# Performance work log

Hardware: AMD Instinct MI355X
Metric: run time of the kernel (lower is better)

The kernel has to match this reference:

```python
import jax, jax.numpy as jnp
import numpy as np

N, S, E = 50000, 16, 400000
D, EDIM = 128, 64
H, K = 4, 32          # n_head, per-head output_dim
NMP, DEPTH = 2, 2


def attn_agg(x, neigh, Wq, Wk, Wv):
    # x: [n, D], neigh: [n, s, D], W*: [H, D, K]
    q = jnp.einsum('nd,hdk->nhk', x, Wq)
    k = jnp.einsum('nsd,hdk->nshk', neigh, Wk)
    v = jnp.einsum('nsd,hdk->nshk', neigh, Wv)
    scale = jnp.asarray(1.0 / np.sqrt(K), x.dtype)
    scores = jnp.einsum('nhk,nshk->nhs', q, k) * scale
    attn = jax.nn.softmax(scores, axis=-1)
    out = jax.nn.elu(jnp.einsum('nhs,nshk->nhk', attn, v))  # activation per head
    return out.reshape(out.shape[0], H * K)                  # concat heads


def setup_inputs():
    key = jax.random.key(0)
    ks = jax.random.split(key, 14)
    sD, sE = 1.0 / np.sqrt(D), 1.0 / np.sqrt(EDIM)
    return {
        'feats': jax.random.normal(ks[0], (N, D), jnp.float32),
        'node_emb': jax.random.normal(ks[1], (N, D), jnp.float32) * 0.02,
        'Wprep': jax.random.normal(ks[2], (D, D), jnp.float32) * sD,
        'edge_emb': jax.random.normal(ks[3], (NMP, E, EDIM), jnp.float32),
        'Wedgeprep': jax.random.normal(ks[4], (NMP, EDIM, D), jnp.float32) * sE,
        'Wq_e': jax.random.normal(ks[5], (NMP, DEPTH, H, D, K), jnp.float32) * sD,
        'Wk_e': jax.random.normal(ks[6], (NMP, DEPTH, H, D, K), jnp.float32) * sD,
        'Wv_e': jax.random.normal(ks[7], (NMP, DEPTH, H, D, K), jnp.float32) * sD,
        'Wq_n': jax.random.normal(ks[8], (NMP, DEPTH, H, D, K), jnp.float32) * sD,
        'Wk_n': jax.random.normal(ks[9], (NMP, DEPTH, H, D, K), jnp.float32) * sD,
        'Wv_n': jax.random.normal(ks[10], (NMP, DEPTH, H, D, K), jnp.float32) * sD,
        'node2edge_idx': jax.random.randint(ks[11], (NMP, N, S), 0, E, jnp.int32),
        'edge_node_adj': jax.random.randint(ks[12], (NMP, E, 2), 0, N, jnp.int32),
    }


def reference(feats, node_emb, Wprep, edge_emb, Wedgeprep,
              Wq_e, Wk_e, Wv_e, Wq_n, Wk_n, Wv_n,
              node2edge_idx, edge_node_adj):
    outputs = []
    for mp in range(NMP):
        f = jax.lax.stop_gradient(feats)           # feats[all_ids].detach()
        dummy_feats = node_emb                      # prep layer_idx=0 (id embedding)
        all_feats = f @ Wprep                       # prep layer_idx=1
        all_edges = edge_emb[mp] @ Wedgeprep[mp]    # edge_prep[mp], shuffle=False
        skip = []
        for l in range(DEPTH):
            # --- edge update: gather 2 endpoint node feats per edge ---
            en = all_feats[edge_node_adj[mp]]       # [E, 2, D]
            next_edges = attn_agg(all_edges, en, Wq_e[mp, l], Wk_e[mp, l], Wv_e[mp, l])
            # --- node update: gather S incident edge feats per node (OLD edges) ---
            x = dummy_feats if l == 0 else all_feats
            ne = all_edges[node2edge_idx[mp]]       # [N, S, D]
            next_feats = attn_agg(x, ne, Wq_n[mp, l], Wk_n[mp, l], Wv_n[mp, l])
            skip.append(next_feats)
            all_feats, all_edges = next_feats, next_edges
        outputs.append(jnp.concatenate(skip, axis=-1))  # [N, DEPTH*H*K]
    return jnp.stack(outputs, axis=0)                   # [NMP, N, DEPTH*H*K]
```

## Files before the change

### kernel.cpp

```cpp
#include <hip/hip_runtime.h>

#define N_NODES 50000
#define S_NEI 16
#define E_EDGES 400000
#define DDIM 128
#define EDIMC 64
#define NMPC 2
#define DEPTHC 2

typedef __attribute__((ext_vector_type(8))) short short8v;
typedef __attribute__((ext_vector_type(4))) float float4v;

__device__ __forceinline__ unsigned short f2bf(float f) {
  unsigned int u = __float_as_uint(f);
  unsigned int r = (u + 0x7fffu + ((u >> 16) & 1u)) >> 16;
  return (unsigned short)r;
}
__device__ __forceinline__ float bf2f(unsigned short h) { return __uint_as_float((unsigned int)h << 16); }
__device__ __forceinline__ float bflo(unsigned int u) { return __uint_as_float(u << 16); }
__device__ __forceinline__ float bfhi(unsigned int u) { return __uint_as_float(u & 0xffff0000u); }

__global__ void build_wt(const float* __restrict__ Wprep, const float* __restrict__ Wedgeprep,
                         const float* __restrict__ Wq_e, const float* __restrict__ Wk_e,
                         const float* __restrict__ Wv_e, const float* __restrict__ Wq_n,
                         const float* __restrict__ Wk_n, const float* __restrict__ Wv_n,
                         unsigned short* __restrict__ WT) {
  int idx = blockIdx.x * 256 + threadIdx.x;
  if (idx >= 27 * 16384) return;
  int slot = idx >> 14, r = idx & 16383;
  float v = 0.f;
  if (slot < 24) {
    int ml = slot / 6, mat = slot % 6;
    int c = r >> 7, d = r & 127;
    int h = c >> 5, kk = c & 31;
    const float* W = (mat == 0) ? Wk_e : (mat == 1) ? Wv_e : (mat == 2) ? Wq_n
                   : (mat == 3) ? Wq_e : (mat == 4) ? Wk_n : Wv_n;
    v = W[(((size_t)ml * 4 + h) * 128 + d) * 32 + kk];
  } else if (slot == 24) {
    int c = r >> 7, d = r & 127;
    v = Wprep[d * 128 + c];
  } else {
    int mp = slot - 25;
    int c = r >> 6, k = r & 63;
    if (c < 128) v = Wedgeprep[((size_t)mp * 64 + k) * 128 + c];
  }
  WT[idx] = f2bf(v);
}

template<int KDIM, int NW, bool ASPLIT>
__global__ __launch_bounds__(256, 3)
void proj(const unsigned short* __restrict__ Xbf, const float* __restrict__ Xf,
          const unsigned short* __restrict__ WT,
          unsigned short* __restrict__ Y0, unsigned short* __restrict__ Y1,
          unsigned short* __restrict__ Y2, int rs0, int rs1, int rs2, int M) {
  constexpr int NKK  = KDIM / 32;
  constexpr int CHPR = KDIM / 8;
  constexpr int SWZ  = CHPR - 1;
  __shared__ unsigned short Wl[128 * KDIM];
  const int tid  = threadIdx.x;
  const int lane = tid & 63;
  const int wv   = tid >> 6;
  const int l15  = lane & 15, lg = lane >> 4;
  const long m0  = (long)blockIdx.x * 128 + wv * 32;

  short8v xb[2][NKK];
  #pragma unroll
  for (int rf = 0; rf < 2; ++rf) {
    long row = m0 + rf * 16 + l15; if (row >= M) row = M - 1;
    #pragma unroll
    for (int kk = 0; kk < NKK; ++kk) {
      const int k0 = kk * 32 + lg * 8;
      if (ASPLIT) {
        const float* p = Xf + row * KDIM + k0;
        float4v a0 = *(const float4v*)p;
        float4v a1 = *(const float4v*)(p + 4);
        #pragma unroll
        for (int j = 0; j < 8; ++j) {
          float x = (j < 4) ? a0[j] : a1[j - 4];
          xb[rf][kk][j] = (short)f2bf(x);
        }
      } else {
        xb[rf][kk] = *(const short8v*)(Xbf + row * KDIM + k0);
      }
    }
  }

  unsigned short* Ys[3] = {Y0, Y1, Y2};
  const int rsv[3] = {rs0, rs1, rs2};
  #pragma unroll
  for (int w = 0; w < NW; ++w) {
    if (w) __syncthreads();
    {
      const uint4* src = (const uint4*)(WT + (size_t)w * 16384);
      #pragma unroll
      for (int i = 0; i < CHPR / 2; ++i) {
        int ci = i * 256 + tid;
        int row = ci / CHPR, ch = ci & SWZ;
        uint4 v = src[ci];
        *(uint4*)((char*)Wl + row * (KDIM * 2) + ((ch ^ (row & SWZ)) << 4)) = v;
      }
    }
    __syncthreads();

    float4v acc[8][2];
    #pragma unroll
    for (int cf = 0; cf < 8; ++cf)
      #pragma unroll
      for (int rf = 0; rf < 2; ++rf) acc[cf][rf] = (float4v)0.f;

    #pragma unroll
    for (int kk = 0; kk < NKK; ++kk) {
      #pragma unroll
      for (int cf = 0; cf < 8; ++cf) {
        const int row = cf * 16 + l15;
        const int ch  = (kk * 4 + lg) ^ (row & SWZ);
        short8v b = *(const short8v*)((char*)Wl + row * (KDIM * 2) + (ch << 4));
        acc[cf][0] = __builtin_amdgcn_mfma_f32_16x16x32_bf16(b, xb[0][kk], acc[cf][0], 0, 0, 0);
        acc[cf][1] = __builtin_amdgcn_mfma_f32_16x16x32_bf16(b, xb[1][kk], acc[cf][1], 0, 0, 0);
      }
    }

    #pragma unroll
    for (int rf = 0; rf < 2; ++rf) {
      const long m = m0 + rf * 16 + l15;
      if (m < M) {
        #pragma unroll
        for (int cf = 0; cf < 8; ++cf) {
          const int c0 = cf * 16 + lg * 4;
          float4v a = acc[cf][rf];
          ushort4 o;
          o.x = f2bf(a[0]); o.y = f2bf(a[1]); o.z = f2bf(a[2]); o.w = f2bf(a[3]);
          *(ushort4*)(Ys[w] + m * (long)rsv[w] + c0) = o;
        }
      }
    }
  }
}

__global__ __launch_bounds__(256, 3)
void edge_fused(unsigned short* __restrict__ ehi, const unsigned short* __restrict__ WTqe,
                const unsigned short* __restrict__ KVn, const int* __restrict__ adj,
                unsigned short* __restrict__ KVe) {
  __shared__ unsigned short Wl[128 * 128];
  const int tid  = threadIdx.x;
  const int lane = tid & 63;
  const int wv   = tid >> 6;
  const int l15  = lane & 15, lg = lane >> 4;
  const long m0  = (long)blockIdx.x * 128 + wv * 32;

  short8v xb[2][4];
  #pragma unroll
  for (int rf = 0; rf < 2; ++rf) {
    const long row = m0 + rf * 16 + l15;
    #pragma unroll
    for (int kk = 0; kk < 4; ++kk)
      xb[rf][kk] = *(const short8v*)(ehi + row * 128 + kk * 32 + lg * 8);
  }

  float4v accQ[8][2];
  const int slot_of[3] = {1, 2, 0};
  #pragma unroll
  for (int ph = 0; ph < 3; ++ph) {
    if (ph) __syncthreads();
    {
      const uint4* src = (const uint4*)(WTqe + (size_t)slot_of[ph] * 16384);
      #pragma unroll
      for (int i = 0; i < 8; ++i) {
        int ci = i * 256 + tid;
        int row = ci >> 4, ch = ci & 15;
        uint4 v = src[ci];
        *(uint4*)((char*)Wl + row * 256 + ((ch ^ (row & 15)) << 4)) = v;
      }
    }
    __syncthreads();

    float4v acc[8][2];
    #pragma unroll
    for (int cf = 0; cf < 8; ++cf)
      #pragma unroll
      for (int rf = 0; rf < 2; ++rf) acc[cf][rf] = (float4v)0.f;

    #pragma unroll
    for (int kk = 0; kk < 4; ++kk) {
      #pragma unroll
      for (int cf = 0; cf < 8; ++cf) {
        const int row = cf * 16 + l15;
        const int ch  = (kk * 4 + lg) ^ (row & 15);
        short8v b = *(const short8v*)((char*)Wl + row * 256 + (ch << 4));
        acc[cf][0] = __builtin_amdgcn_mfma_f32_16x16x32_bf16(b, xb[0][kk], acc[cf][0], 0, 0, 0);
        acc[cf][1] = __builtin_amdgcn_mfma_f32_16x16x32_bf16(b, xb[1][kk], acc[cf][1], 0, 0, 0);
      }
    }

    if (ph < 2) {
      #pragma unroll
      for (int rf = 0; rf < 2; ++rf) {
        const long m = m0 + rf * 16 + l15;
        #pragma unroll
        for (int cf = 0; cf < 8; ++cf) {
          const int c0 = cf * 16 + lg * 4;
          float4v a = acc[cf][rf];
          ushort4 o;
          o.x = f2bf(a[0]); o.y = f2bf(a[1]); o.z = f2bf(a[2]); o.w = f2bf(a[3]);
          *(ushort4*)(KVe + m * 256 + ph * 128 + c0) = o;
        }
      }
    } else {
      #pragma unroll
      for (int cf = 0; cf < 8; ++cf)
        #pragma unroll
        for (int rf = 0; rf < 2; ++rf) accQ[cf][rf] = acc[cf][rf];
    }
  }

  const float scale = 0.17677669529663687f;
  #pragma unroll
  for (int rf = 0; rf < 2; ++rf) {
    const long e = m0 + rf * 16 + l15;
    const int2 nn = *(const int2*)(adj + e * 2);
    const size_t b0 = (size_t)nn.x * 256, b1 = (size_t)nn.y * 256;
    float p0[4] = {0.f, 0.f, 0.f, 0.f}, p1[4] = {0.f, 0.f, 0.f, 0.f};
    #pragma unroll
    for (int cf = 0; cf < 8; ++cf) {
      const int c0 = cf * 16 + lg * 4;
      const int h = cf >> 1;
      ushort4 k0 = *(const ushort4*)(KVn + b0 + c0);
      ushort4 k1 = *(const ushort4*)(KVn + b1 + c0);
      float4v q = accQ[cf][rf];
      p0[h] += q[0] * bf2f(k0.x) + q[1] * bf2f(k0.y) + q[2] * bf2f(k0.z) + q[3] * bf2f(k0.w);
      p1[h] += q[0] * bf2f(k1.x) + q[1] * bf2f(k1.y) + q[2] * bf2f(k1.z) + q[3] * bf2f(k1.w);
    }
    float a0[4], a1[4];
    #pragma unroll
    for (int h = 0; h < 4; ++h) {
      p0[h] += __shfl_xor(p0[h], 16); p0[h] += __shfl_xor(p0[h], 32);
      p1[h] += __shfl_xor(p1[h], 16); p1[h] += __shfl_xor(p1[h], 32);
      const float s0 = p0[h] * scale, s1 = p1[h] * scale;
      const float mx = fmaxf(s0, s1);
      const float e0 = __expf(s0 - mx), e1 = __expf(s1 - mx);
      const float inv = 1.0f / (e0 + e1);
      a0[h] = e0 * inv; a1[h] = e1 * inv;
    }
    #pragma unroll
    for (int cf = 0; cf < 8; ++cf) {
      const int c0 = cf * 16 + lg * 4;
      const int h = cf >> 1;
      ushort4 v0 = *(const ushort4*)(KVn + b0 + 128 + c0);
      ushort4 v1 = *(const ushort4*)(KVn + b1 + 128 + c0);
      float o[4];
      o[0] = a0[h] * bf2f(v0.x) + a1[h] * bf2f(v1.x);
      o[1] = a0[h] * bf2f(v0.y) + a1[h] * bf2f(v1.y);
      o[2] = a0[h] * bf2f(v0.z) + a1[h] * bf2f(v1.z);
      o[3] = a0[h] * bf2f(v0.w) + a1[h] * bf2f(v1.w);
      ushort4 ob;
      o[0] = o[0] > 0.f ? o[0] : expm1f(o[0]);
      o[1] = o[1] > 0.f ? o[1] : expm1f(o[1]);
      o[2] = o[2] > 0.f ? o[2] : expm1f(o[2]);
      o[3] = o[3] > 0.f ? o[3] : expm1f(o[3]);
      ob.x = f2bf(o[0]); ob.y = f2bf(o[1]); ob.z = f2bf(o[2]); ob.w = f2bf(o[3]);
      *(ushort4*)(ehi + e * 128 + c0) = ob;
    }
  }
}

__global__ __launch_bounds__(256)
void node_attn(const unsigned int* __restrict__ Qn, const unsigned int* __restrict__ KVe,
               const int* __restrict__ n2e,
               unsigned short* __restrict__ fhi, float* __restrict__ outp) {
  const int lane = threadIdx.x & 63;
  const long n = (long)blockIdx.x * 4 + (threadIdx.x >> 6);
  const unsigned int q = Qn[n * 64 + lane];
  const float qa = bflo(q), qb = bfhi(q);
  float sc[16];
  unsigned int vv[16];
  #pragma unroll
  for (int s = 0; s < 16; ++s) {
    const long e = n2e[n * 16 + s];
    const unsigned int kk = KVe[e * 128 + lane];
    vv[s] = KVe[e * 128 + 64 + lane];
    float p = qa * bflo(kk) + qb * bfhi(kk);
    #pragma unroll
    for (int off = 1; off < 16; off <<= 1) p += __shfl_xor(p, off);
    sc[s] = p * 0.17677669529663687f;
  }
  float m = sc[0];
  #pragma unroll
  for (int s = 1; s < 16; ++s) m = fmaxf(m, sc[s]);
  float sum = 0.f;
  #pragma unroll
  for (int s = 0; s < 16; ++s) { sc[s] = __expf(sc[s] - m); sum += sc[s]; }
  const float inv = 1.0f / sum;
  float oa = 0.f, ob = 0.f;
  #pragma unroll
  for (int s = 0; s < 16; ++s) { oa += sc[s] * bflo(vv[s]); ob += sc[s] * bfhi(vv[s]); }
  oa *= inv; ob *= inv;
  oa = oa > 0.f ? oa : expm1f(oa);
  ob = ob > 0.f ? ob : expm1f(ob);
  ((unsigned int*)fhi)[n * 64 + lane] = (unsigned int)f2bf(oa) | ((unsigned int)f2bf(ob) << 16);
  *(float2*)(outp + n * 256 + lane * 2) = make_float2(oa, ob);
}

extern "C" void kernel_launch(void* const* d_in, const int* in_sizes, int n_in,
                              void* d_out, int out_size, void* d_ws, size_t ws_size,
                              hipStream_t stream) {
  const float* feats     = (const float*)d_in[0];
  const float* node_emb  = (const float*)d_in[1];
  const float* Wprep     = (const float*)d_in[2];
  const float* edge_emb  = (const float*)d_in[3];
  const float* Wedgeprep = (const float*)d_in[4];
  const float* Wq_e      = (const float*)d_in[5];
  const float* Wk_e      = (const float*)d_in[6];
  const float* Wv_e      = (const float*)d_in[7];
  const float* Wq_n      = (const float*)d_in[8];
  const float* Wk_n      = (const float*)d_in[9];
  const float* Wv_n      = (const float*)d_in[10];
  const int*   n2e       = (const int*)d_in[11];
  const int*   adj       = (const int*)d_in[12];
  float* out = (float*)d_out;

  char* w = (char*)d_ws;
  auto carve = [&](size_t bytes) -> char* {
    char* p = w; w += (bytes + 255) & ~(size_t)255; return p;
  };
  unsigned short* ehi  = (unsigned short*)carve((size_t)E_EDGES * 128 * 2);
  unsigned short* fahi = (unsigned short*)carve((size_t)N_NODES * 128 * 2);
  unsigned short* fbhi = (unsigned short*)carve((size_t)N_NODES * 128 * 2);
  unsigned short* KVe  = (unsigned short*)carve((size_t)E_EDGES * 256 * 2);
  unsigned short* KVn  = (unsigned short*)carve((size_t)N_NODES * 256 * 2);
  unsigned short* Qn   = (unsigned short*)carve((size_t)N_NODES * 128 * 2);
  unsigned short* WT   = (unsigned short*)carve((size_t)27 * 16384 * 2);

  build_wt<<<(27 * 16384 + 255) / 256, 256, 0, stream>>>(
      Wprep, Wedgeprep, Wq_e, Wk_e, Wv_e, Wq_n, Wk_n, Wv_n, WT);

  const int gN = (N_NODES + 127) / 128;
  const int gE = E_EDGES / 128;

  for (int mp = 0; mp < NMPC; ++mp) {
    proj<128, 1, true><<<gN, 256, 0, stream>>>(
        nullptr, feats, WT + (size_t)24 * 16384, fahi, nullptr, nullptr, 128, 0, 0, N_NODES);
    proj<64, 1, true><<<gE, 256, 0, stream>>>(
        nullptr, edge_emb + (size_t)mp * E_EDGES * EDIMC,
        WT + (size_t)(25 + mp) * 16384, ehi, nullptr, nullptr, 128, 0, 0, E_EDGES);

    unsigned short *fchi = fahi, *fnhi = fbhi;
    for (int l = 0; l < DEPTHC; ++l) {
      const int ml = mp * 2 + l;
      const unsigned short* base = WT + (size_t)ml * 6 * 16384;
      if (l == 0) {
        proj<128, 2, false><<<gN, 256, 0, stream>>>(
            fchi, nullptr, base, KVn, KVn + 128, nullptr, 256, 256, 0, N_NODES);
        proj<128, 1, true><<<gN, 256, 0, stream>>>(
            nullptr, node_emb, base + (size_t)2 * 16384, Qn, nullptr, nullptr, 128, 0, 0, N_NODES);
      } else {
        proj<128, 3, false><<<gN, 256, 0, stream>>>(
            fchi, nullptr, base, KVn, KVn + 128, Qn, 256, 256, 128, N_NODES);
      }
      edge_fused<<<gE, 256, 0, stream>>>(
          ehi, base + (size_t)3 * 16384, KVn, adj + (size_t)mp * E_EDGES * 2, KVe);
      node_attn<<<N_NODES / 4, 256, 0, stream>>>(
          (const unsigned int*)Qn, (const unsigned int*)KVe,
          n2e + (size_t)mp * N_NODES * S_NEI, fnhi,
          out + (size_t)mp * N_NODES * 256 + (size_t)l * 128);

      unsigned short* t = fchi; fchi = fnhi; fnhi = t;
    }
  }
}
```

Measured before the change: 1.305 ms.

## Split edge kernel into KV-projection and Q-attention block roles with double-buffered edges

The fused edge kernel now launches twice as many blocks: even blocks compute the edge K/V projections and odd blocks compute the Q projection plus the two-endpoint attention. Edge features are ping-ponged between two buffers so the attention blocks can write new edges while the K/V blocks still read the old ones. The node feature prep projection is hoisted out of the message-passing loop into a separate buffer, so it runs once instead of once per mp. This trades one more edge-sized buffer and a duplicated load of the input edge tile for more parallelism and fewer serial phases per block.

Result: slower. 1.556 ms (+19.3%).

```diff
diff --git a/kernel.cpp b/kernel.cpp
--- a/kernel.cpp
+++ b/kernel.cpp
@@ -138,15 +138,16 @@
 }
 
 __global__ __launch_bounds__(256, 3)
-void edge_fused(unsigned short* __restrict__ ehi, const unsigned short* __restrict__ WTqe,
+void edge_layer(const unsigned short* __restrict__ ecur, const unsigned short* __restrict__ WTqe,
                 const unsigned short* __restrict__ KVn, const int* __restrict__ adj,
-                unsigned short* __restrict__ KVe) {
+                unsigned short* __restrict__ KVe, unsigned short* __restrict__ enext) {
   __shared__ unsigned short Wl[128 * 128];
   const int tid  = threadIdx.x;
   const int lane = tid & 63;
   const int wv   = tid >> 6;
   const int l15  = lane & 15, lg = lane >> 4;
-  const long m0  = (long)blockIdx.x * 128 + wv * 32;
+  const int role = blockIdx.x & 1;
+  const long m0  = (long)(blockIdx.x >> 1) * 128 + wv * 32;
 
   short8v xb[2][4];
   #pragma unroll
@@ -154,45 +155,43 @@
     const long row = m0 + rf * 16 + l15;
     #pragma unroll
     for (int kk = 0; kk < 4; ++kk)
-      xb[rf][kk] = *(const short8v*)(ehi + row * 128 + kk * 32 + lg * 8);
-  }
-
-  float4v accQ[8][2];
-  const int slot_of[3] = {1, 2, 0};
-  #pragma unroll
-  for (int ph = 0; ph < 3; ++ph) {
-    if (ph) __syncthreads();
-    {
-      const uint4* src = (const uint4*)(WTqe + (size_t)slot_of[ph] * 16384);
-      #pragma unroll
-      for (int i = 0; i < 8; ++i) {
-        int ci = i * 256 + tid;
-        int row = ci >> 4, ch = ci & 15;
-        uint4 v = src[ci];
-        *(uint4*)((char*)Wl + row * 256 + ((ch ^ (row & 15)) << 4)) = v;
-      }
-    }
-    __syncthreads();
-
-    float4v acc[8][2];
-    #pragma unroll
-    for (int cf = 0; cf < 8; ++cf)
-      #pragma unroll
-      for (int rf = 0; rf < 2; ++rf) acc[cf][rf] = (float4v)0.f;
-
-    #pragma unroll
-    for (int kk = 0; kk < 4; ++kk) {
-      #pragma unroll
-      for (int cf = 0; cf < 8; ++cf) {
-        const int row = cf * 16 + l15;
-        const int ch  = (kk * 4 + lg) ^ (row & 15);
-        short8v b = *(const short8v*)((char*)Wl + row * 256 + (ch << 4));
-        acc[cf][0] = __builtin_amdgcn_mfma_f32_16x16x32_bf16(b, xb[0][kk], acc[cf][0], 0, 0, 0);
-        acc[cf][1] = __builtin_amdgcn_mfma_f32_16x16x32_bf16(b, xb[1][kk], acc[cf][1], 0, 0, 0);
-      }
-    }
-
-    if (ph < 2) {
+      xb[rf][kk] = *(const short8v*)(ecur + row * 128 + kk * 32 + lg * 8);
+  }
+
+  if (role == 0) {
+    #pragma unroll
+    for (int ph = 0; ph < 2; ++ph) {
+      if (ph) __syncthreads();
+      {
+        const uint4* src = (const uint4*)(WTqe + (size_t)(ph + 1) * 16384);
+        #pragma unroll
+        for (int i = 0; i < 8; ++i) {
+          int ci = i * 256 + tid;
+          int row = ci >> 4, ch = ci & 15;
+          uint4 v = src[ci];
+          *(uint4*)((char*)Wl + row * 256 + ((ch ^ (row & 15)) << 4)) = v;
+        }
+      }
+      __syncthreads();
+
+      float4v acc[8][2];
+      #pragma unroll
+      for (int cf = 0; cf < 8; ++cf)
+        #pragma unroll
+        for (int rf = 0; rf < 2; ++rf) acc[cf][rf] = (float4v)0.f;
+
+      #pragma unroll
+      for (int kk = 0; kk < 4; ++kk) {
+        #pragma unroll
+        for (int cf = 0; cf < 8; ++cf) {
+          const int row = cf * 16 + l15;
+          const int ch  = (kk * 4 + lg) ^ (row & 15);
+          short8v b = *(const short8v*)((char*)Wl + row * 256 + (ch << 4));
+          acc[cf][0] = __builtin_amdgcn_mfma_f32_16x16x32_bf16(b, xb[0][kk], acc[cf][0], 0, 0, 0);
+          acc[cf][1] = __builtin_amdgcn_mfma_f32_16x16x32_bf16(b, xb[1][kk], acc[cf][1], 0, 0, 0);
+        }
+      }
+
       #pragma unroll
       for (int rf = 0; rf < 2; ++rf) {
         const long m = m0 + rf * 16 + l15;
@@ -205,11 +204,37 @@
           *(ushort4*)(KVe + m * 256 + ph * 128 + c0) = o;
         }
       }
-    } else {
-      #pragma unroll
-      for (int cf = 0; cf < 8; ++cf)
-        #pragma unroll
-        for (int rf = 0; rf < 2; ++rf) accQ[cf][rf] = acc[cf][rf];
+    }
+    return;
+  }
+
+  {
+    const uint4* src = (const uint4*)WTqe;
+    #pragma unroll
+    for (int i = 0; i < 8; ++i) {
+      int ci = i * 256 + tid;
+      int row = ci >> 4, ch = ci & 15;
+      uint4 v = src[ci];
+      *(uint4*)((char*)Wl + row * 256 + ((ch ^ (row & 15)) << 4)) = v;
+    }
+  }
+  __syncthreads();
+
+  float4v accQ[8][2];
+  #pragma unroll
+  for (int cf = 0; cf < 8; ++cf)
+    #pragma unroll
+    for (int rf = 0; rf < 2; ++rf) accQ[cf][rf] = (float4v)0.f;
+
+  #pragma unroll
+  for (int kk = 0; kk < 4; ++kk) {
+    #pragma unroll
+    for (int cf = 0; cf < 8; ++cf) {
+      const int row = cf * 16 + l15;
+      const int ch  = (kk * 4 + lg) ^ (row & 15);
+      short8v b = *(const short8v*)((char*)Wl + row * 256 + (ch << 4));
+      accQ[cf][0] = __builtin_amdgcn_mfma_f32_16x16x32_bf16(b, xb[0][kk], accQ[cf][0], 0, 0, 0);
+      accQ[cf][1] = __builtin_amdgcn_mfma_f32_16x16x32_bf16(b, xb[1][kk], accQ[cf][1], 0, 0, 0);
     }
   }
 
@@ -252,13 +277,13 @@
       o[1] = a0[h] * bf2f(v0.y) + a1[h] * bf2f(v1.y);
       o[2] = a0[h] * bf2f(v0.z) + a1[h] * bf2f(v1.z);
       o[3] = a0[h] * bf2f(v0.w) + a1[h] * bf2f(v1.w);
-      ushort4 ob;
       o[0] = o[0] > 0.f ? o[0] : expm1f(o[0]);
       o[1] = o[1] > 0.f ? o[1] : expm1f(o[1]);
       o[2] = o[2] > 0.f ? o[2] : expm1f(o[2]);
       o[3] = o[3] > 0.f ? o[3] : expm1f(o[3]);
+      ushort4 ob;
       ob.x = f2bf(o[0]); ob.y = f2bf(o[1]); ob.z = f2bf(o[2]); ob.w = f2bf(o[3]);
-      *(ushort4*)(ehi + e * 128 + c0) = ob;
+      *(ushort4*)(enext + e * 128 + c0) = ob;
     }
   }
 }
@@ -322,13 +347,15 @@
   auto carve = [&](size_t bytes) -> char* {
     char* p = w; w += (bytes + 255) & ~(size_t)255; return p;
   };
-  unsigned short* ehi  = (unsigned short*)carve((size_t)E_EDGES * 128 * 2);
-  unsigned short* fahi = (unsigned short*)carve((size_t)N_NODES * 128 * 2);
-  unsigned short* fbhi = (unsigned short*)carve((size_t)N_NODES * 128 * 2);
-  unsigned short* KVe  = (unsigned short*)carve((size_t)E_EDGES * 256 * 2);
-  unsigned short* KVn  = (unsigned short*)carve((size_t)N_NODES * 256 * 2);
-  unsigned short* Qn   = (unsigned short*)carve((size_t)N_NODES * 128 * 2);
-  unsigned short* WT   = (unsigned short*)carve((size_t)27 * 16384 * 2);
+  unsigned short* e_a   = (unsigned short*)carve((size_t)E_EDGES * 128 * 2);
+  unsigned short* e_b   = (unsigned short*)carve((size_t)E_EDGES * 128 * 2);
+  unsigned short* fprep = (unsigned short*)carve((size_t)N_NODES * 128 * 2);
+  unsigned short* fa    = (unsigned short*)carve((size_t)N_NODES * 128 * 2);
+  unsigned short* fb    = (unsigned short*)carve((size_t)N_NODES * 128 * 2);
+  unsigned short* KVe   = (unsigned short*)carve((size_t)E_EDGES * 256 * 2);
+  unsigned short* KVn   = (unsigned short*)carve((size_t)N_NODES * 256 * 2);
+  unsigned short* Qn    = (unsigned short*)carve((size_t)N_NODES * 128 * 2);
+  unsigned short* WT    = (unsigned short*)carve((size_t)27 * 16384 * 2);
 
   build_wt<<<(27 * 16384 + 255) / 256, 256, 0, stream>>>(
       Wprep, Wedgeprep, Wq_e, Wk_e, Wv_e, Wq_n, Wk_n, Wv_n, WT);
@@ -336,14 +363,16 @@
   const int gN = (N_NODES + 127) / 128;
   const int gE = E_EDGES / 128;
 
+  proj<128, 1, true><<<gN, 256, 0, stream>>>(
+      nullptr, feats, WT + (size_t)24 * 16384, fprep, nullptr, nullptr, 128, 0, 0, N_NODES);
+
   for (int mp = 0; mp < NMPC; ++mp) {
-    proj<128, 1, true><<<gN, 256, 0, stream>>>(
-        nullptr, feats, WT + (size_t)24 * 16384, fahi, nullptr, nullptr, 128, 0, 0, N_NODES);
     proj<64, 1, true><<<gE, 256, 0, stream>>>(
         nullptr, edge_emb + (size_t)mp * E_EDGES * EDIMC,
-        WT + (size_t)(25 + mp) * 16384, ehi, nullptr, nullptr, 128, 0, 0, E_EDGES);
-
-    unsigned short *fchi = fahi, *fnhi = fbhi;
+        WT + (size_t)(25 + mp) * 16384, e_a, nullptr, nullptr, 128, 0, 0, E_EDGES);
+
+    unsigned short *ecur = e_a, *enext = e_b;
+    unsigned short *fchi = fprep, *fnhi = fa;
     for (int l = 0; l < DEPTHC; ++l) {
       const int ml = mp * 2 + l;
       const unsigned short* base = WT + (size_t)ml * 6 * 16384;
@@ -356,14 +385,15 @@
         proj<128, 3, false><<<gN, 256, 0, stream>>>(
             fchi, nullptr, base, KVn, KVn + 128, Qn, 256, 256, 128, N_NODES);
       }
-      edge_fused<<<gE, 256, 0, stream>>>(
-          ehi, base + (size_t)3 * 16384, KVn, adj + (size_t)mp * E_EDGES * 2, KVe);
+      edge_layer<<<2 * gE, 256, 0, stream>>>(
+          ecur, base + (size_t)3 * 16384, KVn, adj + (size_t)mp * E_EDGES * 2, KVe, enext);
       node_attn<<<N_NODES / 4, 256, 0, stream>>>(
           (const unsigned int*)Qn, (const unsigned int*)KVe,
           n2e + (size_t)mp * N_NODES * S_NEI, fnhi,
           out + (size_t)mp * N_NODES * 256 + (size_t)l * 128);
 
-      unsigned short* t = fchi; fchi = fnhi; fnhi = t;
-    }
-  }
-}
+      unsigned short* t = ecur; ecur = enext; enext = t;
+      fchi = fnhi; fnhi = fb;
+    }
+  }
+}
```

## Stage edge queries in LDS and gather endpoint K/V with coalesced per-edge rows

Applied to the files above, without the earlier changes.

The edge attention epilogue writes the MFMA query accumulators to swizzled shared memory, then processes one edge per wavefront iteration. Each lane reads one 32-bit bf16 pair of K/V from the two endpoint rows, so the gathers become contiguous 256-byte row reads instead of scattered 8-byte fragments. The shuffle reduction now runs within 16-lane head groups. Separately, the node prep projection (feats @ Wprep), identical for both message-passing passes, is hoisted out of the mp loop into its own buffer, saving one N×128 GEMM. The cost is an extra LDS round trip and barrier, and a serial 32-iteration loop per wave.

Result: slower. 1.361 ms (+4.3%).

```diff
diff --git a/kernel.cpp b/kernel.cpp
--- a/kernel.cpp
+++ b/kernel.cpp
@@ -213,53 +213,50 @@
     }
   }
 
+  __syncthreads();
+  #pragma unroll
+  for (int rf = 0; rf < 2; ++rf) {
+    const int er = wv * 32 + rf * 16 + l15;
+    #pragma unroll
+    for (int cf = 0; cf < 8; ++cf) {
+      const int cb = (cf * 32 + lg * 8) ^ ((er & 15) << 4);
+      float4v a = accQ[cf][rf];
+      ushort4 o;
+      o.x = f2bf(a[0]); o.y = f2bf(a[1]); o.z = f2bf(a[2]); o.w = f2bf(a[3]);
+      *(ushort4*)((char*)Wl + er * 256 + cb) = o;
+    }
+  }
+
   const float scale = 0.17677669529663687f;
-  #pragma unroll
-  for (int rf = 0; rf < 2; ++rf) {
-    const long e = m0 + rf * 16 + l15;
+  #pragma unroll 2
+  for (int i = 0; i < 32; ++i) {
+    const int er = wv * 32 + i;
+    const long e = (long)blockIdx.x * 128 + er;
     const int2 nn = *(const int2*)(adj + e * 2);
-    const size_t b0 = (size_t)nn.x * 256, b1 = (size_t)nn.y * 256;
-    float p0[4] = {0.f, 0.f, 0.f, 0.f}, p1[4] = {0.f, 0.f, 0.f, 0.f};
-    #pragma unroll
-    for (int cf = 0; cf < 8; ++cf) {
-      const int c0 = cf * 16 + lg * 4;
-      const int h = cf >> 1;
-      ushort4 k0 = *(const ushort4*)(KVn + b0 + c0);
-      ushort4 k1 = *(const ushort4*)(KVn + b1 + c0);
-      float4v q = accQ[cf][rf];
-      p0[h] += q[0] * bf2f(k0.x) + q[1] * bf2f(k0.y) + q[2] * bf2f(k0.z) + q[3] * bf2f(k0.w);
-      p1[h] += q[0] * bf2f(k1.x) + q[1] * bf2f(k1.y) + q[2] * bf2f(k1.z) + q[3] * bf2f(k1.w);
-    }
-    float a0[4], a1[4];
-    #pragma unroll
-    for (int h = 0; h < 4; ++h) {
-      p0[h] += __shfl_xor(p0[h], 16); p0[h] += __shfl_xor(p0[h], 32);
-      p1[h] += __shfl_xor(p1[h], 16); p1[h] += __shfl_xor(p1[h], 32);
-      const float s0 = p0[h] * scale, s1 = p1[h] * scale;
-      const float mx = fmaxf(s0, s1);
-      const float e0 = __expf(s0 - mx), e1 = __expf(s1 - mx);
-      const float inv = 1.0f / (e0 + e1);
-      a0[h] = e0 * inv; a1[h] = e1 * inv;
-    }
-    #pragma unroll
-    for (int cf = 0; cf < 8; ++cf) {
-      const int c0 = cf * 16 + lg * 4;
-      const int h = cf >> 1;
-      ushort4 v0 = *(const ushort4*)(KVn + b0 + 128 + c0);
-      ushort4 v1 = *(const ushort4*)(KVn + b1 + 128 + c0);
-      float o[4];
-      o[0] = a0[h] * bf2f(v0.x) + a1[h] * bf2f(v1.x);
-      o[1] = a0[h] * bf2f(v0.y) + a1[h] * bf2f(v1.y);
-      o[2] = a0[h] * bf2f(v0.z) + a1[h] * bf2f(v1.z);
-      o[3] = a0[h] * bf2f(v0.w) + a1[h] * bf2f(v1.w);
-      ushort4 ob;
-      o[0] = o[0] > 0.f ? o[0] : expm1f(o[0]);
-      o[1] = o[1] > 0.f ? o[1] : expm1f(o[1]);
-      o[2] = o[2] > 0.f ? o[2] : expm1f(o[2]);
-      o[3] = o[3] > 0.f ? o[3] : expm1f(o[3]);
-      ob.x = f2bf(o[0]); ob.y = f2bf(o[1]); ob.z = f2bf(o[2]); ob.w = f2bf(o[3]);
-      *(ushort4*)(ehi + e * 128 + c0) = ob;
-    }
+    const unsigned int q =
+        *(const unsigned int*)((char*)Wl + er * 256 + ((lane * 4) ^ ((er & 15) << 4)));
+    const unsigned int* R0 = (const unsigned int*)(KVn + (size_t)nn.x * 256);
+    const unsigned int* R1 = (const unsigned int*)(KVn + (size_t)nn.y * 256);
+    const unsigned int k0 = R0[lane], v0 = R0[64 + lane];
+    const unsigned int k1 = R1[lane], v1 = R1[64 + lane];
+    const float qa = bflo(q), qb = bfhi(q);
+    float p0 = qa * bflo(k0) + qb * bfhi(k0);
+    float p1 = qa * bflo(k1) + qb * bfhi(k1);
+    #pragma unroll
+    for (int off = 1; off < 16; off <<= 1) {
+      p0 += __shfl_xor(p0, off);
+      p1 += __shfl_xor(p1, off);
+    }
+    const float s0 = p0 * scale, s1 = p1 * scale;
+    const float mx = fmaxf(s0, s1);
+    const float e0 = __expf(s0 - mx), e1 = __expf(s1 - mx);
+    const float inv = 1.0f / (e0 + e1);
+    const float a0 = e0 * inv, a1 = e1 * inv;
+    float oa = a0 * bflo(v0) + a1 * bflo(v1);
+    float ob = a0 * bfhi(v0) + a1 * bfhi(v1);
+    oa = oa > 0.f ? oa : expm1f(oa);
+    ob = ob > 0.f ? ob : expm1f(ob);
+    ((unsigned int*)ehi)[e * 64 + lane] = (unsigned int)f2bf(oa) | ((unsigned int)f2bf(ob) << 16);
   }
 }
 
@@ -322,13 +319,14 @@
   auto carve = [&](size_t bytes) -> char* {
     char* p = w; w += (bytes + 255) & ~(size_t)255; return p;
   };
-  unsigned short* ehi  = (unsigned short*)carve((size_t)E_EDGES * 128 * 2);
-  unsigned short* fahi = (unsigned short*)carve((size_t)N_NODES * 128 * 2);
-  unsigned short* fbhi = (unsigned short*)carve((size_t)N_NODES * 128 * 2);
-  unsigned short* KVe  = (unsigned short*)carve((size_t)E_EDGES * 256 * 2);
-  unsigned short* KVn  = (unsigned short*)carve((size_t)N_NODES * 256 * 2);
-  unsigned short* Qn   = (unsigned short*)carve((size_t)N_NODES * 128 * 2);
-  unsigned short* WT   = (unsigned short*)carve((size_t)27 * 16384 * 2);
+  unsigned short* ehi   = (unsigned short*)carve((size_t)E_EDGES * 128 * 2);
+  unsigned short* fprep = (unsigned short*)carve((size_t)N_NODES * 128 * 2);
+  unsigned short* fa    = (unsigned short*)carve((size_t)N_NODES * 128 * 2);
+  unsigned short* fb    = (unsigned short*)carve((size_t)N_NODES * 128 * 2);
+  unsigned short* KVe   = (unsigned short*)carve((size_t)E_EDGES * 256 * 2);
+  unsigned short* KVn   = (unsigned short*)carve((size_t)N_NODES * 256 * 2);
+  unsigned short* Qn    = (unsigned short*)carve((size_t)N_NODES * 128 * 2);
+  unsigned short* WT    = (unsigned short*)carve((size_t)27 * 16384 * 2);
 
   build_wt<<<(27 * 16384 + 255) / 256, 256, 0, stream>>>(
       Wprep, Wedgeprep, Wq_e, Wk_e, Wv_e, Wq_n, Wk_n, Wv_n, WT);
@@ -336,14 +334,15 @@
   const int gN = (N_NODES + 127) / 128;
   const int gE = E_EDGES / 128;
 
+  proj<128, 1, true><<<gN, 256, 0, stream>>>(
+      nullptr, feats, WT + (size_t)24 * 16384, fprep, nullptr, nullptr, 128, 0, 0, N_NODES);
+
   for (int mp = 0; mp < NMPC; ++mp) {
-    proj<128, 1, true><<<gN, 256, 0, stream>>>(
-        nullptr, feats, WT + (size_t)24 * 16384, fahi, nullptr, nullptr, 128, 0, 0, N_NODES);
     proj<64, 1, true><<<gE, 256, 0, stream>>>(
         nullptr, edge_emb + (size_t)mp * E_EDGES * EDIMC,
         WT + (size_t)(25 + mp) * 16384, ehi, nullptr, nullptr, 128, 0, 0, E_EDGES);
 
-    unsigned short *fchi = fahi, *fnhi = fbhi;
+    unsigned short *fchi = fprep, *fnhi = fa;
     for (int l = 0; l < DEPTHC; ++l) {
       const int ml = mp * 2 + l;
       const unsigned short* base = WT + (size_t)ml * 6 * 16384;
@@ -363,7 +362,7 @@
           n2e + (size_t)mp * N_NODES * S_NEI, fnhi,
           out + (size_t)mp * N_NODES * 256 + (size_t)l * 128);
 
-      unsigned short* t = fchi; fchi = fnhi; fnhi = t;
-    }
-  }
-}
+      fchi = fnhi; fnhi = fb;
+    }
+  }
+}
```
